# Kernel tuning notes

Hardware: AMD Instinct MI355X
Metric: run time of the kernel (lower is better)

## Reference

```python
import jax, jax.numpy as jnp
import numpy as np

NUM_HEADS = 8
NUM_GROUPS = 32
EPS = 1e-5


def setup_inputs() -> dict:
    key = jax.random.key(0)
    ks = jax.random.split(key, 12)
    B, C, H, W = 8, 512, 32, 32
    E = 512
    s = 1.0 / np.sqrt(C)
    inp = {
        "input_tensor": jax.random.normal(ks[0], (B, C, H, W), dtype=jnp.float32),
        "Wq": jax.random.normal(ks[1], (C, E), dtype=jnp.float32) * s,
        "bq": jnp.zeros((E,), dtype=jnp.float32),
        "Wk": jax.random.normal(ks[2], (C, E), dtype=jnp.float32) * s,
        "bk": jnp.zeros((E,), dtype=jnp.float32),
        "Wv": jax.random.normal(ks[3], (C, E), dtype=jnp.float32) * s,
        "bv": jnp.zeros((E,), dtype=jnp.float32),
        "Wo": jax.random.normal(ks[4], (E, E), dtype=jnp.float32) * s,
        "bo": jnp.zeros((E,), dtype=jnp.float32),
        "gamma": jnp.ones((E,), dtype=jnp.float32),
        "beta": jnp.zeros((E,), dtype=jnp.float32),
    }
    return inp


def reference(input_tensor, Wq, bq, Wk, bk, Wv, bv, Wo, bo, gamma, beta):
    B, C, H, W = input_tensor.shape
    E = Wq.shape[1]
    nH = NUM_HEADS
    hd = E // nH
    S = H * W

    # [B, C, H, W] -> [B, S, C]
    x = input_tensor.reshape(B, C, S).transpose(0, 2, 1)

    q = (x @ Wq + bq).reshape(B, S, nH, hd).transpose(0, 2, 1, 3)  # [B, h, S, d]
    k = (x @ Wk + bk).reshape(B, S, nH, hd).transpose(0, 2, 1, 3)
    v = (x @ Wv + bv).reshape(B, S, nH, hd).transpose(0, 2, 1, 3)

    scale = hd ** (-0.5)
    scores = jnp.einsum("bhqd,bhkd->bhqk", q, k) * scale
    weights = jax.nn.softmax(scores, axis=-1)
    attn = jnp.einsum("bhqk,bhkd->bhqd", weights, v)  # [B, h, S, d]

    attn = attn.transpose(0, 2, 1, 3).reshape(B, S, E)
    out = attn @ Wo + bo  # [B, S, E]
    out = out.transpose(0, 2, 1).reshape(B, E, H, W)

    y = out + input_tensor

    # GroupNorm over (channels_per_group, H, W)
    G = NUM_GROUPS
    yg = y.reshape(B, G, E // G, H, W)
    mean = jnp.mean(yg, axis=(2, 3, 4), keepdims=True)
    var = jnp.var(yg, axis=(2, 3, 4), keepdims=True)
    yn = ((yg - mean) * jax.lax.rsqrt(var + EPS)).reshape(B, E, H, W)
    return yn * gamma[None, :, None, None] + beta[None, :, None, None]
```

## Files before the change

kernel.cpp:

```cpp
#include <hip/hip_runtime.h>
#include <math.h>

constexpr int Bn  = 8;
constexpr int Cc  = 512;
constexpr int Ss  = 1024;
constexpr int Ee  = 512;
constexpr int nHd = 8;
constexpr int Hd  = 64;
constexpr int Gg  = 32;
constexpr int Cpg = 16;

typedef __bf16 bf16x8 __attribute__((ext_vector_type(8)));
typedef float  f32x4  __attribute__((ext_vector_type(4)));
typedef float  f32x16 __attribute__((ext_vector_type(16)));
typedef unsigned u32x4 __attribute__((ext_vector_type(4)));

__device__ inline __bf16 cvt_bf16(float f) {
    unsigned u = __builtin_bit_cast(unsigned, f);
    u += 0x7fffu + ((u >> 16) & 1u);
    unsigned short h = (unsigned short)(u >> 16);
    return __builtin_bit_cast(__bf16, h);
}

__device__ inline void gld16(const __bf16* g, __bf16* l) {
    __builtin_amdgcn_global_load_lds(
        (const __attribute__((address_space(1))) void*)g,
        (__attribute__((address_space(3))) void*)l, 16, 0, 0);
}

__device__ inline unsigned pk_bf16_rtz(float hi, float lo) {
    return __builtin_amdgcn_perm(__builtin_bit_cast(unsigned, hi),
                                 __builtin_bit_cast(unsigned, lo), 0x07060302u);
}

__global__ __launch_bounds__(256) void transpose_xw(
    const float* __restrict__ x, __bf16* __restrict__ xt,
    const float* __restrict__ w0, const float* __restrict__ w1,
    const float* __restrict__ w2, const float* __restrict__ w3,
    __bf16* __restrict__ d0, __bf16* __restrict__ d1,
    __bf16* __restrict__ d2, __bf16* __restrict__ d3,
    float* __restrict__ stats)
{
    __shared__ float T[32][33];
    const int r8 = threadIdx.x >> 5, c32 = threadIdx.x & 31;
    const int z = blockIdx.z;
    if (z < 8) {
        const int b = z, c0 = blockIdx.y * 32, s0 = blockIdx.x * 32;
#pragma unroll
        for (int i = 0; i < 4; i++)
            T[r8 + i * 8][c32] =
                x[((size_t)b * Cc + c0 + r8 + i * 8) * Ss + s0 + c32];
        __syncthreads();
#pragma unroll
        for (int i = 0; i < 4; i++)
            xt[((size_t)b * Ss + s0 + r8 + i * 8) * Cc + c0 + c32] =
                cvt_bf16(T[c32][r8 + i * 8]);
    } else {
        if (z == 8 && blockIdx.x == 0 && blockIdx.y == 0) {
            stats[threadIdx.x] = 0.0f;
            stats[threadIdx.x + 256] = 0.0f;
        }
        if (blockIdx.x >= 16) return;
        const int m = z - 8;
        const float* src = (m == 0) ? w0 : (m == 1) ? w1 : (m == 2) ? w2 : w3;
        __bf16* dst = (m == 0) ? d0 : (m == 1) ? d1 : (m == 2) ? d2 : d3;
        const int e0 = blockIdx.x * 32, c0 = blockIdx.y * 32;
#pragma unroll
        for (int i = 0; i < 4; i++)
            T[r8 + i * 8][c32] = src[(size_t)(c0 + r8 + i * 8) * Ee + e0 + c32];
        __syncthreads();
#pragma unroll
        for (int i = 0; i < 4; i++)
            dst[(size_t)(e0 + r8 + i * 8) * Cc + c0 + c32] =
                cvt_bf16(T[c32][r8 + i * 8]);
    }
}

__global__ __launch_bounds__(256) void qkv_mfma(
    const __bf16* __restrict__ xt,
    const __bf16* __restrict__ wqt, const __bf16* __restrict__ wkt,
    const __bf16* __restrict__ wvt,
    const float* __restrict__ bq, const float* __restrict__ bk,
    const float* __restrict__ bv,
    __bf16* __restrict__ qb, __bf16* __restrict__ kb, __bf16* __restrict__ vt)
{
    const int b = blockIdx.z;
    const int wsel = blockIdx.y >> 2;
    const int e0 = (blockIdx.y & 3) * 128;
    const int s0 = blockIdx.x * 128;
    const __bf16* A  = xt + (size_t)b * Ss * Cc;
    const __bf16* Bm = (wsel == 0) ? wqt : (wsel == 1) ? wkt : wvt;
    const float*  bias = (wsel == 0) ? bq : (wsel == 1) ? bk : bv;

    __shared__ __align__(16) char smem[128 * 136 * 2];
    __bf16* T = (__bf16*)smem;

    const int wave = threadIdx.x >> 6, lane = threadIdx.x & 63;
    const int lid = lane & 15, quad = lane >> 4;
    const int wm = wave & 1, wn = wave >> 1;
    const int srow = lane >> 2, sch = lane & 3;

    f32x4 acc[4][4] = {};

    auto stage = [&](int k0, int bufi) {
        __bf16* Asb = (__bf16*)(smem + bufi * 16384);
        __bf16* Bsb = (__bf16*)(smem + bufi * 16384 + 8192);
#pragma unroll
        for (int i = 0; i < 2; i++) {
            const int inst = wave * 2 + i;
            const int r = inst * 16 + srow;
            gld16(&A [(size_t)(s0 + r) * Cc + k0 + sch * 8], &Asb[inst * 512]);
            gld16(&Bm[(size_t)(e0 + r) * Cc + k0 + sch * 8], &Bsb[inst * 512]);
        }
    };

    stage(0, 0);
    for (int it = 0; it < 16; it++) {
        __syncthreads();
        if (it + 1 < 16) stage((it + 1) * 32, (it + 1) & 1);
        const __bf16* Asb = (const __bf16*)(smem + (it & 1) * 16384);
        const __bf16* Bsb = Asb + 4096;
        bf16x8 af[4], bf[4];
#pragma unroll
        for (int i = 0; i < 4; i++)
            af[i] = *(const bf16x8*)&Asb[(wm * 64 + i * 16 + lid) * 32 + quad * 8];
#pragma unroll
        for (int j = 0; j < 4; j++)
            bf[j] = *(const bf16x8*)&Bsb[(wn * 64 + j * 16 + lid) * 32 + quad * 8];
#pragma unroll
        for (int i = 0; i < 4; i++)
#pragma unroll
            for (int j = 0; j < 4; j++)
                acc[i][j] = __builtin_amdgcn_mfma_f32_16x16x32_bf16(
                    af[i], bf[j], acc[i][j], 0, 0, 0);
    }
    __syncthreads();

    float bj[4];
#pragma unroll
    for (int j = 0; j < 4; j++) bj[j] = bias[e0 + wn * 64 + j * 16 + lid];

    if (wsel == 2) {
#pragma unroll
        for (int i = 0; i < 4; i++) {
            const int s4 = wm * 64 + i * 16 + quad * 4;
#pragma unroll
            for (int j = 0; j < 4; j++) {
                const int e_l = wn * 64 + j * 16 + lid;
                unsigned short u0 = __builtin_bit_cast(unsigned short, cvt_bf16(acc[i][j][0] + bj[j]));
                unsigned short u1 = __builtin_bit_cast(unsigned short, cvt_bf16(acc[i][j][1] + bj[j]));
                unsigned short u2 = __builtin_bit_cast(unsigned short, cvt_bf16(acc[i][j][2] + bj[j]));
                unsigned short u3 = __builtin_bit_cast(unsigned short, cvt_bf16(acc[i][j][3] + bj[j]));
                uint2 pk;
                pk.x = (unsigned)u0 | ((unsigned)u1 << 16);
                pk.y = (unsigned)u2 | ((unsigned)u3 << 16);
                *(uint2*)&T[e_l * 136 + s4] = pk;
            }
        }
        __syncthreads();
        const int t = threadIdx.x;
#pragma unroll
        for (int it = 0; it < 8; it++) {
            const int idx = t + it * 256;
            const int e_l = idx >> 4, c8 = (idx & 15) * 8;
            bf16x8 val = *(const bf16x8*)&T[e_l * 136 + c8];
            const int e_g = e0 + e_l;
            const int head = e_g >> 6, d = e_g & 63;
            *(bf16x8*)&vt[(((size_t)b * nHd + head) * Hd + d) * Ss + s0 + c8] = val;
        }
    } else {
        __bf16* outp = (wsel == 0) ? qb : kb;
#pragma unroll
        for (int i = 0; i < 4; i++) {
#pragma unroll
            for (int j = 0; j < 4; j++) {
                const int e1 = e0 + wn * 64 + j * 16 + lid;
                const int head = e1 >> 6, d = e1 & 63;
#pragma unroll
                for (int r = 0; r < 4; r++) {
                    const int s1 = s0 + wm * 64 + i * 16 + quad * 4 + r;
                    outp[(((size_t)b * nHd + head) * Ss + s1) * Hd + d] =
                        cvt_bf16(acc[i][j][r] + bj[j]);
                }
            }
        }
    }
}

__global__ __launch_bounds__(256, 2) void attn_mfma(
    const __bf16* __restrict__ q, const __bf16* __restrict__ k,
    const __bf16* __restrict__ vt, __bf16* __restrict__ attn_out)
{
    const int bh = blockIdx.x;
    const int s0 = blockIdx.y * 128;
    const __bf16* qp = q  + (size_t)bh * Ss * Hd;
    const __bf16* kp = k  + (size_t)bh * Ss * Hd;
    const __bf16* vp = vt + (size_t)bh * Hd * Ss;

    __shared__ __align__(16) __bf16 Ks[2][128 * 64];
    __shared__ __align__(16) __bf16 Vs[2][64 * 128];

    const int wave = threadIdx.x >> 6, lane = threadIdx.x & 63;
    const int nl = lane & 31, h = lane >> 5;

    const int sq = s0 + wave * 32 + nl;
    bf16x8 qf[4];
#pragma unroll
    for (int kk2 = 0; kk2 < 4; kk2++)
        qf[kk2] = *(const bf16x8*)&qp[(size_t)sq * Hd + kk2 * 16 + h * 8];

    f32x16 oacc[2] = {};
    float rs = 0.0f;
    const float cexp = 0.125f * 1.44269504f;

    const int srow8 = lane >> 3, sch8 = lane & 7;
    const int srow4 = lane >> 4, sch16 = lane & 15;

    auto stageKV = [&](int kt, int bufi) {
        __bf16* Ksb = Ks[bufi];
        __bf16* Vsb = Vs[bufi];
#pragma unroll
        for (int i = 0; i < 4; i++) {
            const int inst = wave * 4 + i;
            const int rK = inst * 8 + srow8;
            gld16(&kp[(size_t)(kt * 128 + rK) * Hd + ((sch8 ^ (rK & 7)) * 8)],
                  &Ksb[inst * 512]);
            const int dR = inst * 4 + srow4;
            gld16(&vp[(size_t)dR * Ss + kt * 128 + ((sch16 ^ (dR & 15)) * 8)],
                  &Vsb[inst * 512]);
        }
    };

    stageKV(0, 0);
    for (int kt = 0; kt < 8; kt++) {
        __syncthreads();
        if (kt + 1 < 8) stageKV(kt + 1, (kt + 1) & 1);
        const __bf16* Ksb = Ks[kt & 1];
        const __bf16* Vsb = Vs[kt & 1];

        f32x16 sc[4] = {};
#pragma unroll
        for (int kk2 = 0; kk2 < 4; kk2++) {
#pragma unroll
            for (int mt = 0; mt < 4; mt++) {
                bf16x8 kf = *(const bf16x8*)&Ksb[(mt * 32 + nl) * 64 +
                                                 (((2 * kk2 + h) ^ (nl & 7)) * 8)];
                sc[mt] = __builtin_amdgcn_mfma_f32_32x32x16_bf16(
                    kf, qf[kk2], sc[mt], 0, 0, 0);
            }
        }

        unsigned frag[8][4];
#pragma unroll
        for (int mt = 0; mt < 4; mt++) {
            float p[16];
#pragma unroll
            for (int r = 0; r < 16; r++) {
                p[r] = __builtin_amdgcn_exp2f(sc[mt][r] * cexp);
                rs += p[r];
            }
            unsigned G[4][2];
#pragma unroll
            for (int qg = 0; qg < 4; qg++) {
                G[qg][0] = pk_bf16_rtz(p[4 * qg + 1], p[4 * qg + 0]);
                G[qg][1] = pk_bf16_rtz(p[4 * qg + 3], p[4 * qg + 2]);
            }
            const unsigned sA0 = h ? G[0][0] : G[1][0];
            const unsigned sA1 = h ? G[0][1] : G[1][1];
            const unsigned sB0 = h ? G[2][0] : G[3][0];
            const unsigned sB1 = h ? G[2][1] : G[3][1];
            const unsigned rA0 = __shfl_xor(sA0, 32, 64);
            const unsigned rA1 = __shfl_xor(sA1, 32, 64);
            const unsigned rB0 = __shfl_xor(sB0, 32, 64);
            const unsigned rB1 = __shfl_xor(sB1, 32, 64);
            frag[2 * mt][0]     = h ? rA0     : G[0][0];
            frag[2 * mt][1]     = h ? rA1     : G[0][1];
            frag[2 * mt][2]     = h ? G[1][0] : rA0;
            frag[2 * mt][3]     = h ? G[1][1] : rA1;
            frag[2 * mt + 1][0] = h ? rB0     : G[2][0];
            frag[2 * mt + 1][1] = h ? rB1     : G[2][1];
            frag[2 * mt + 1][2] = h ? G[3][0] : rB0;
            frag[2 * mt + 1][3] = h ? G[3][1] : rB1;
        }

#pragma unroll
        for (int kk = 0; kk < 8; kk++) {
            u32x4 fv = {frag[kk][0], frag[kk][1], frag[kk][2], frag[kk][3]};
            bf16x8 pf = __builtin_bit_cast(bf16x8, fv);
#pragma unroll
            for (int dt = 0; dt < 2; dt++) {
                bf16x8 vf = *(const bf16x8*)&Vsb[(dt * 32 + nl) * 128 +
                                                 (((kk * 2 + h) ^ (nl & 15)) * 8)];
                oacc[dt] = __builtin_amdgcn_mfma_f32_32x32x16_bf16(
                    pf, vf, oacc[dt], 0, 0, 0);
            }
        }
    }

    rs += __shfl_xor(rs, 32, 64);
    const float inv = 1.0f / rs;
    const int b = bh >> 3, head = bh & 7;
#pragma unroll
    for (int r = 0; r < 16; r++) {
        const int rowq = (r & 3) + 8 * (r >> 2) + 4 * h;
        const float invr = __shfl(inv, rowq, 64);
        const int s1 = s0 + wave * 32 + rowq;
#pragma unroll
        for (int dt = 0; dt < 2; dt++)
            attn_out[((size_t)b * Ss + s1) * Ee + head * Hd + dt * 32 + nl] =
                cvt_bf16(oacc[dt][r] * invr);
    }
}

__global__ __launch_bounds__(256) void outproj_mfma(
    const __bf16* __restrict__ attnb, const __bf16* __restrict__ wot,
    const float* __restrict__ bo, const float* __restrict__ xin,
    __bf16* __restrict__ y, float* __restrict__ stats)
{
    const int b  = blockIdx.z;
    const int e0 = blockIdx.y * 128;
    const int s0 = blockIdx.x * 128;
    const __bf16* Bm = attnb + (size_t)b * Ss * Ee;

    __shared__ __align__(16) char smem[32768];

    const int wave = threadIdx.x >> 6, lane = threadIdx.x & 63;
    const int lid = lane & 15, quad = lane >> 4;
    const int wm = wave & 1, wn = wave >> 1;
    const int srow = lane >> 2, sch = lane & 3;

    f32x4 acc[4][4] = {};

    auto stage = [&](int k0, int bufi) {
        __bf16* Asb = (__bf16*)(smem + bufi * 16384);
        __bf16* Bsb = (__bf16*)(smem + bufi * 16384 + 8192);
#pragma unroll
        for (int i = 0; i < 2; i++) {
            const int inst = wave * 2 + i;
            const int r = inst * 16 + srow;
            gld16(&wot[(size_t)(e0 + r) * Ee + k0 + sch * 8], &Asb[inst * 512]);
            gld16(&Bm [(size_t)(s0 + r) * Ee + k0 + sch * 8], &Bsb[inst * 512]);
        }
    };

    stage(0, 0);
    for (int it = 0; it < 16; it++) {
        __syncthreads();
        if (it + 1 < 16) stage((it + 1) * 32, (it + 1) & 1);
        const __bf16* Asb = (const __bf16*)(smem + (it & 1) * 16384);
        const __bf16* Bsb = Asb + 4096;
        bf16x8 af[4], bf[4];
#pragma unroll
        for (int i = 0; i < 4; i++)
            af[i] = *(const bf16x8*)&Asb[(wm * 64 + i * 16 + lid) * 32 + quad * 8];
#pragma unroll
        for (int j = 0; j < 4; j++)
            bf[j] = *(const bf16x8*)&Bsb[(wn * 64 + j * 16 + lid) * 32 + quad * 8];
#pragma unroll
        for (int i = 0; i < 4; i++)
#pragma unroll
            for (int j = 0; j < 4; j++)
                acc[i][j] = __builtin_amdgcn_mfma_f32_16x16x32_bf16(
                    af[i], bf[j], acc[i][j], 0, 0, 0);
    }

    float gs[4] = {}, gs2[4] = {};
#pragma unroll
    for (int i = 0; i < 4; i++) {
#pragma unroll
        for (int r = 0; r < 4; r++) {
            const int eo1 = e0 + wm * 64 + i * 16 + quad * 4 + r;
            const float bb = bo[eo1];
#pragma unroll
            for (int j = 0; j < 4; j++) {
                const int s1 = s0 + wn * 64 + j * 16 + lid;
                const size_t idx = ((size_t)b * Ee + eo1) * Ss + s1;
                const float v = acc[i][j][r] + bb + xin[idx];
                y[idx] = cvt_bf16(v);
                gs[i]  += v;
                gs2[i] += v * v;
            }
        }
    }
#pragma unroll
    for (int i = 0; i < 4; i++) {
        float a = gs[i], c = gs2[i];
#pragma unroll
        for (int off = 32; off > 0; off >>= 1) {
            a += __shfl_down(a, off, 64);
            c += __shfl_down(c, off, 64);
        }
        if (lane == 0) {
            const int g = (e0 >> 4) + wm * 4 + i;
            atomicAdd(&stats[(b * Gg + g) * 2 + 0], a);
            atomicAdd(&stats[(b * Gg + g) * 2 + 1], c);
        }
    }
}

__global__ __launch_bounds__(256) void gnorm_kernel(
    const __bf16* __restrict__ y, const float* __restrict__ gamma,
    const float* __restrict__ beta, const float* __restrict__ stats,
    float* __restrict__ out)
{
    const int bg = blockIdx.x;
    const int b = bg >> 5, g = bg & 31;
    const size_t base = ((size_t)b * Ee + g * Cpg) * Ss;
    const bf16x8* y8 = (const bf16x8*)(y + base);
    constexpr int N8 = (Cpg * Ss) / 8;
    constexpr float Nf = (float)(Cpg * Ss);

    const float mean = stats[bg * 2 + 0] / Nf;
    const float var  = stats[bg * 2 + 1] / Nf - mean * mean;
    const float rstd = rsqrtf(var + 1e-5f);

    for (int i = threadIdx.x; i < N8; i += 256) {
        bf16x8 vv = y8[i];
        const int c = g * Cpg + (i >> 7);
        const float gm = gamma[c] * rstd;
        const float bt = beta[c];
        f32x4 r0, r1;
#pragma unroll
        for (int j = 0; j < 4; j++) r0[j] = ((float)vv[j] - mean) * gm + bt;
#pragma unroll
        for (int j = 0; j < 4; j++) r1[j] = ((float)vv[4 + j] - mean) * gm + bt;
        *(f32x4*)&out[base + (size_t)i * 8]     = r0;
        *(f32x4*)&out[base + (size_t)i * 8 + 4] = r1;
    }
}

extern "C" void kernel_launch(void* const* d_in, const int* in_sizes, int n_in,
                              void* d_out, int out_size, void* d_ws, size_t ws_size,
                              hipStream_t stream)
{
    const float* x     = (const float*)d_in[0];
    const float* Wq    = (const float*)d_in[1];
    const float* bq    = (const float*)d_in[2];
    const float* Wk    = (const float*)d_in[3];
    const float* bk    = (const float*)d_in[4];
    const float* Wv    = (const float*)d_in[5];
    const float* bv    = (const float*)d_in[6];
    const float* Wo    = (const float*)d_in[7];
    const float* bo    = (const float*)d_in[8];
    const float* gamma = (const float*)d_in[9];
    const float* beta  = (const float*)d_in[10];
    float* out = (float*)d_out;

    char* ws = (char*)d_ws;
    __bf16* xt    = (__bf16*)ws;
    __bf16* wqt   = (__bf16*)(ws + (8u << 20));
    __bf16* wkt   = (__bf16*)(ws + (8u << 20) + (512u << 10));
    __bf16* wvt   = (__bf16*)(ws + (9u << 20));
    __bf16* wot   = (__bf16*)(ws + (9u << 20) + (512u << 10));
    __bf16* qb    = (__bf16*)(ws + (10u << 20));
    __bf16* kb    = (__bf16*)(ws + (18u << 20));
    __bf16* vtb   = (__bf16*)(ws + (26u << 20));
    __bf16* attnb = (__bf16*)(ws + (34u << 20));
    __bf16* yb    = (__bf16*)(ws + (42u << 20));
    float*  statb = (float*) (ws + (50u << 20));

    transpose_xw<<<dim3(32, 16, 12), 256, 0, stream>>>(
        x, xt, Wq, Wk, Wv, Wo, wqt, wkt, wvt, wot, statb);

    qkv_mfma<<<dim3(Ss / 128, 12, Bn), 256, 0, stream>>>(
        xt, wqt, wkt, wvt, bq, bk, bv, qb, kb, vtb);

    attn_mfma<<<dim3(Bn * nHd, Ss / 128), 256, 0, stream>>>(qb, kb, vtb, attnb);

    outproj_mfma<<<dim3(Ss / 128, Ee / 128, Bn), 256, 0, stream>>>(
        attnb, wot, bo, x, yb, statb);

    gnorm_kernel<<<Bn * Gg, 256, 0, stream>>>(yb, gamma, beta, statb, out);
}
```

Measured before the change: 155.9 us.

## Fuse GroupNorm into out-projection via grid-level counter barrier per group slice

The separate GroupNorm kernel and the bf16 intermediate y buffer are removed. Each out-projection block keeps its residual-added values in registers and atomically accumulates group statistics. It then waits on a per-(batch, channel-tile) counter until all 8 spatial blocks have contributed, reads the final mean and variance, and writes normalized fp32 output directly. This saves a full write and read of y plus one kernel launch. It relies on all 8 cooperating blocks being co-resident, since the spin-wait would deadlock otherwise; with 256 blocks that is likely but not guaranteed.

```diff
diff --git a/kernel.cpp b/kernel.cpp
--- a/kernel.cpp
+++ b/kernel.cpp
@@ -39,7 +39,7 @@
     const float* __restrict__ w2, const float* __restrict__ w3,
     __bf16* __restrict__ d0, __bf16* __restrict__ d1,
     __bf16* __restrict__ d2, __bf16* __restrict__ d3,
-    float* __restrict__ stats)
+    float* __restrict__ stats, unsigned* __restrict__ cnt)
 {
     __shared__ float T[32][33];
     const int r8 = threadIdx.x >> 5, c32 = threadIdx.x & 31;
@@ -59,6 +59,7 @@
         if (z == 8 && blockIdx.x == 0 && blockIdx.y == 0) {
             stats[threadIdx.x] = 0.0f;
             stats[threadIdx.x + 256] = 0.0f;
+            if (threadIdx.x < 32) cnt[threadIdx.x] = 0u;
         }
         if (blockIdx.x >= 16) return;
         const int m = z - 8;
@@ -312,10 +313,12 @@
     }
 }
 
-__global__ __launch_bounds__(256) void outproj_mfma(
+__global__ __launch_bounds__(256) void outproj_gnorm(
     const __bf16* __restrict__ attnb, const __bf16* __restrict__ wot,
     const float* __restrict__ bo, const float* __restrict__ xin,
-    __bf16* __restrict__ y, float* __restrict__ stats)
+    const float* __restrict__ gamma, const float* __restrict__ beta,
+    float* __restrict__ stats, unsigned* __restrict__ cnt,
+    float* __restrict__ out)
 {
     const int b  = blockIdx.z;
     const int e0 = blockIdx.y * 128;
@@ -376,7 +379,7 @@
                 const int s1 = s0 + wn * 64 + j * 16 + lid;
                 const size_t idx = ((size_t)b * Ee + eo1) * Ss + s1;
                 const float v = acc[i][j][r] + bb + xin[idx];
-                y[idx] = cvt_bf16(v);
+                acc[i][j][r] = v;
                 gs[i]  += v;
                 gs2[i] += v * v;
             }
@@ -396,36 +399,44 @@
             atomicAdd(&stats[(b * Gg + g) * 2 + 1], c);
         }
     }
-}
-
-__global__ __launch_bounds__(256) void gnorm_kernel(
-    const __bf16* __restrict__ y, const float* __restrict__ gamma,
-    const float* __restrict__ beta, const float* __restrict__ stats,
-    float* __restrict__ out)
-{
-    const int bg = blockIdx.x;
-    const int b = bg >> 5, g = bg & 31;
-    const size_t base = ((size_t)b * Ee + g * Cpg) * Ss;
-    const bf16x8* y8 = (const bf16x8*)(y + base);
-    constexpr int N8 = (Cpg * Ss) / 8;
+
+    __threadfence();
+    const int ci = b * 4 + (e0 >> 7);
+    if (threadIdx.x == 0) {
+        atomicAdd(&cnt[ci], 1u);
+        while (atomicAdd(&cnt[ci], 0u) < 8u) __builtin_amdgcn_s_sleep(2);
+    }
+    __syncthreads();
+
+    __shared__ float gmean[8], grstd[8];
     constexpr float Nf = (float)(Cpg * Ss);
-
-    const float mean = stats[bg * 2 + 0] / Nf;
-    const float var  = stats[bg * 2 + 1] / Nf - mean * mean;
-    const float rstd = rsqrtf(var + 1e-5f);
-
-    for (int i = threadIdx.x; i < N8; i += 256) {
-        bf16x8 vv = y8[i];
-        const int c = g * Cpg + (i >> 7);
-        const float gm = gamma[c] * rstd;
-        const float bt = beta[c];
-        f32x4 r0, r1;
-#pragma unroll
-        for (int j = 0; j < 4; j++) r0[j] = ((float)vv[j] - mean) * gm + bt;
-#pragma unroll
-        for (int j = 0; j < 4; j++) r1[j] = ((float)vv[4 + j] - mean) * gm + bt;
-        *(f32x4*)&out[base + (size_t)i * 8]     = r0;
-        *(f32x4*)&out[base + (size_t)i * 8 + 4] = r1;
+    if (threadIdx.x < 8) {
+        const int g = (e0 >> 4) + threadIdx.x;
+        const float sum = atomicAdd(&stats[(b * Gg + g) * 2 + 0], 0.0f);
+        const float sq  = atomicAdd(&stats[(b * Gg + g) * 2 + 1], 0.0f);
+        const float mean = sum / Nf;
+        const float var  = sq / Nf - mean * mean;
+        gmean[threadIdx.x] = mean;
+        grstd[threadIdx.x] = rsqrtf(var + 1e-5f);
+    }
+    __syncthreads();
+
+#pragma unroll
+    for (int i = 0; i < 4; i++) {
+        const float mean = gmean[wm * 4 + i];
+        const float rstd = grstd[wm * 4 + i];
+#pragma unroll
+        for (int r = 0; r < 4; r++) {
+            const int eo1 = e0 + wm * 64 + i * 16 + quad * 4 + r;
+            const float gm = gamma[eo1] * rstd;
+            const float bt = beta[eo1];
+#pragma unroll
+            for (int j = 0; j < 4; j++) {
+                const int s1 = s0 + wn * 64 + j * 16 + lid;
+                const size_t idx = ((size_t)b * Ee + eo1) * Ss + s1;
+                out[idx] = (acc[i][j][r] - mean) * gm + bt;
+            }
+        }
     }
 }
 
@@ -456,19 +467,17 @@
     __bf16* kb    = (__bf16*)(ws + (18u << 20));
     __bf16* vtb   = (__bf16*)(ws + (26u << 20));
     __bf16* attnb = (__bf16*)(ws + (34u << 20));
-    __bf16* yb    = (__bf16*)(ws + (42u << 20));
-    float*  statb = (float*) (ws + (50u << 20));
+    float*  statb = (float*) (ws + (42u << 20));
+    unsigned* cntb = (unsigned*)(ws + (42u << 20) + 2048);
 
     transpose_xw<<<dim3(32, 16, 12), 256, 0, stream>>>(
-        x, xt, Wq, Wk, Wv, Wo, wqt, wkt, wvt, wot, statb);
+        x, xt, Wq, Wk, Wv, Wo, wqt, wkt, wvt, wot, statb, cntb);
 
     qkv_mfma<<<dim3(Ss / 128, 12, Bn), 256, 0, stream>>>(
         xt, wqt, wkt, wvt, bq, bk, bv, qb, kb, vtb);
 
     attn_mfma<<<dim3(Bn * nHd, Ss / 128), 256, 0, stream>>>(qb, kb, vtb, attnb);
 
-    outproj_mfma<<<dim3(Ss / 128, Ee / 128, Bn), 256, 0, stream>>>(
-        attnb, wot, bo, x, yb, statb);
-
-    gnorm_kernel<<<Bn * Gg, 256, 0, stream>>>(yb, gamma, beta, statb, out);
-}
+    outproj_gnorm<<<dim3(Ss / 128, Ee / 128, Bn), 256, 0, stream>>>(
+        attnb, wot, bo, x, gamma, beta, statb, cntb, out);
+}
```

After: 174.8 us. 1.12x slower.

## Fuse Q/K/V projections into one 512-thread block sharing the X tile

Applied to the files above, without the earlier changes.

The QKV GEMM kernel now computes Q, K and V for the same 128x128 output tile in one block of 512 threads, instead of launching separate blocks per weight matrix. Each block stages the shared X tile once along with all three weight tiles, which removes the repeated reads of X and cuts the grid to a third of its former size. In exchange each block uses 64KB of shared memory and 96 accumulator registers per lane, which may lower occupancy. The block count drops from 768 to 256, which may hurt load balance across CUs.

```diff
diff --git a/kernel.cpp b/kernel.cpp
--- a/kernel.cpp
+++ b/kernel.cpp
@@ -76,7 +76,7 @@
     }
 }
 
-__global__ __launch_bounds__(256) void qkv_mfma(
+__global__ __launch_bounds__(512, 2) void qkv_mfma(
     const __bf16* __restrict__ xt,
     const __bf16* __restrict__ wqt, const __bf16* __restrict__ wkt,
     const __bf16* __restrict__ wvt,
@@ -84,33 +84,34 @@
     const float* __restrict__ bv,
     __bf16* __restrict__ qb, __bf16* __restrict__ kb, __bf16* __restrict__ vt)
 {
-    const int b = blockIdx.z;
-    const int wsel = blockIdx.y >> 2;
-    const int e0 = (blockIdx.y & 3) * 128;
+    const int b  = blockIdx.z;
+    const int e0 = blockIdx.y * 128;
     const int s0 = blockIdx.x * 128;
-    const __bf16* A  = xt + (size_t)b * Ss * Cc;
-    const __bf16* Bm = (wsel == 0) ? wqt : (wsel == 1) ? wkt : wvt;
-    const float*  bias = (wsel == 0) ? bq : (wsel == 1) ? bk : bv;
-
-    __shared__ __align__(16) char smem[128 * 136 * 2];
-    __bf16* T = (__bf16*)smem;
+    const __bf16* A = xt + (size_t)b * Ss * Cc;
+
+    __shared__ __align__(16) char smem[65536];
 
     const int wave = threadIdx.x >> 6, lane = threadIdx.x & 63;
     const int lid = lane & 15, quad = lane >> 4;
     const int wm = wave & 1, wn = wave >> 1;
     const int srow = lane >> 2, sch = lane & 3;
 
-    f32x4 acc[4][4] = {};
+    const int mat = wave >> 1;
+    const __bf16* msrc =
+        (mat == 0) ? (A   + (size_t)s0 * Cc) :
+        (mat == 1) ? (wqt + (size_t)e0 * Cc) :
+        (mat == 2) ? (wkt + (size_t)e0 * Cc) : (wvt + (size_t)e0 * Cc);
+    const int rbase = (wave & 1) * 64;
+
+    f32x4 acc[3][4][2] = {};
 
     auto stage = [&](int k0, int bufi) {
-        __bf16* Asb = (__bf16*)(smem + bufi * 16384);
-        __bf16* Bsb = (__bf16*)(smem + bufi * 16384 + 8192);
-#pragma unroll
-        for (int i = 0; i < 2; i++) {
-            const int inst = wave * 2 + i;
-            const int r = inst * 16 + srow;
-            gld16(&A [(size_t)(s0 + r) * Cc + k0 + sch * 8], &Asb[inst * 512]);
-            gld16(&Bm[(size_t)(e0 + r) * Cc + k0 + sch * 8], &Bsb[inst * 512]);
+        __bf16* base = (__bf16*)(smem + bufi * 32768);
+#pragma unroll
+        for (int i = 0; i < 4; i++) {
+            const int r = rbase + i * 16 + srow;
+            gld16(&msrc[(size_t)r * Cc + k0 + sch * 8],
+                  &base[(wave * 4 + i) * 512]);
         }
     };
 
@@ -118,69 +119,80 @@
     for (int it = 0; it < 16; it++) {
         __syncthreads();
         if (it + 1 < 16) stage((it + 1) * 32, (it + 1) & 1);
-        const __bf16* Asb = (const __bf16*)(smem + (it & 1) * 16384);
-        const __bf16* Bsb = Asb + 4096;
-        bf16x8 af[4], bf[4];
-#pragma unroll
-        for (int i = 0; i < 4; i++)
-            af[i] = *(const bf16x8*)&Asb[(wm * 64 + i * 16 + lid) * 32 + quad * 8];
-#pragma unroll
-        for (int j = 0; j < 4; j++)
-            bf[j] = *(const bf16x8*)&Bsb[(wn * 64 + j * 16 + lid) * 32 + quad * 8];
-#pragma unroll
-        for (int i = 0; i < 4; i++)
-#pragma unroll
-            for (int j = 0; j < 4; j++)
-                acc[i][j] = __builtin_amdgcn_mfma_f32_16x16x32_bf16(
-                    af[i], bf[j], acc[i][j], 0, 0, 0);
+        const __bf16* buf = (const __bf16*)(smem + (it & 1) * 32768);
+        bf16x8 af[4];
+#pragma unroll
+        for (int i = 0; i < 4; i++)
+            af[i] = *(const bf16x8*)&buf[(wm * 64 + i * 16 + lid) * 32 + quad * 8];
+#pragma unroll
+        for (int w = 0; w < 3; w++) {
+            const __bf16* Bs = buf + 4096 * (w + 1);
+            bf16x8 bf0 = *(const bf16x8*)&Bs[(wn * 32 + lid) * 32 + quad * 8];
+            bf16x8 bf1 = *(const bf16x8*)&Bs[(wn * 32 + 16 + lid) * 32 + quad * 8];
+#pragma unroll
+            for (int i = 0; i < 4; i++) {
+                acc[w][i][0] = __builtin_amdgcn_mfma_f32_16x16x32_bf16(
+                    af[i], bf0, acc[w][i][0], 0, 0, 0);
+                acc[w][i][1] = __builtin_amdgcn_mfma_f32_16x16x32_bf16(
+                    af[i], bf1, acc[w][i][1], 0, 0, 0);
+            }
+        }
     }
     __syncthreads();
 
-    float bj[4];
-#pragma unroll
-    for (int j = 0; j < 4; j++) bj[j] = bias[e0 + wn * 64 + j * 16 + lid];
-
-    if (wsel == 2) {
-#pragma unroll
-        for (int i = 0; i < 4; i++) {
-            const int s4 = wm * 64 + i * 16 + quad * 4;
-#pragma unroll
-            for (int j = 0; j < 4; j++) {
-                const int e_l = wn * 64 + j * 16 + lid;
-                unsigned short u0 = __builtin_bit_cast(unsigned short, cvt_bf16(acc[i][j][0] + bj[j]));
-                unsigned short u1 = __builtin_bit_cast(unsigned short, cvt_bf16(acc[i][j][1] + bj[j]));
-                unsigned short u2 = __builtin_bit_cast(unsigned short, cvt_bf16(acc[i][j][2] + bj[j]));
-                unsigned short u3 = __builtin_bit_cast(unsigned short, cvt_bf16(acc[i][j][3] + bj[j]));
-                uint2 pk;
-                pk.x = (unsigned)u0 | ((unsigned)u1 << 16);
-                pk.y = (unsigned)u2 | ((unsigned)u3 << 16);
-                *(uint2*)&T[e_l * 136 + s4] = pk;
-            }
-        }
-        __syncthreads();
+    const float* biasArr[3] = {bq, bk, bv};
+    float bj[3][2];
+#pragma unroll
+    for (int w = 0; w < 3; w++)
+#pragma unroll
+        for (int j = 0; j < 2; j++)
+            bj[w][j] = biasArr[w][e0 + wn * 32 + j * 16 + lid];
+
+    __bf16* T = (__bf16*)smem;
+#pragma unroll
+    for (int i = 0; i < 4; i++) {
+        const int s4 = wm * 64 + i * 16 + quad * 4;
+#pragma unroll
+        for (int j = 0; j < 2; j++) {
+            const int e_l = wn * 32 + j * 16 + lid;
+            unsigned short u0 = __builtin_bit_cast(unsigned short, cvt_bf16(acc[2][i][j][0] + bj[2][j]));
+            unsigned short u1 = __builtin_bit_cast(unsigned short, cvt_bf16(acc[2][i][j][1] + bj[2][j]));
+            unsigned short u2 = __builtin_bit_cast(unsigned short, cvt_bf16(acc[2][i][j][2] + bj[2][j]));
+            unsigned short u3 = __builtin_bit_cast(unsigned short, cvt_bf16(acc[2][i][j][3] + bj[2][j]));
+            uint2 pk;
+            pk.x = (unsigned)u0 | ((unsigned)u1 << 16);
+            pk.y = (unsigned)u2 | ((unsigned)u3 << 16);
+            *(uint2*)&T[e_l * 136 + s4] = pk;
+        }
+    }
+    __syncthreads();
+    {
         const int t = threadIdx.x;
 #pragma unroll
-        for (int it = 0; it < 8; it++) {
-            const int idx = t + it * 256;
+        for (int it2 = 0; it2 < 4; it2++) {
+            const int idx = t + it2 * 512;
             const int e_l = idx >> 4, c8 = (idx & 15) * 8;
             bf16x8 val = *(const bf16x8*)&T[e_l * 136 + c8];
             const int e_g = e0 + e_l;
             const int head = e_g >> 6, d = e_g & 63;
             *(bf16x8*)&vt[(((size_t)b * nHd + head) * Hd + d) * Ss + s0 + c8] = val;
         }
-    } else {
-        __bf16* outp = (wsel == 0) ? qb : kb;
+    }
+
+#pragma unroll
+    for (int w = 0; w < 2; w++) {
+        __bf16* outp = w ? kb : qb;
 #pragma unroll
         for (int i = 0; i < 4; i++) {
 #pragma unroll
-            for (int j = 0; j < 4; j++) {
-                const int e1 = e0 + wn * 64 + j * 16 + lid;
+            for (int j = 0; j < 2; j++) {
+                const int e1 = e0 + wn * 32 + j * 16 + lid;
                 const int head = e1 >> 6, d = e1 & 63;
 #pragma unroll
                 for (int r = 0; r < 4; r++) {
                     const int s1 = s0 + wm * 64 + i * 16 + quad * 4 + r;
                     outp[(((size_t)b * nHd + head) * Ss + s1) * Hd + d] =
-                        cvt_bf16(acc[i][j][r] + bj[j]);
+                        cvt_bf16(acc[w][i][j][r] + bj[w][j]);
                 }
             }
         }
@@ -462,7 +474,7 @@
     transpose_xw<<<dim3(32, 16, 12), 256, 0, stream>>>(
         x, xt, Wq, Wk, Wv, Wo, wqt, wkt, wvt, wot, statb);
 
-    qkv_mfma<<<dim3(Ss / 128, 12, Bn), 256, 0, stream>>>(
+    qkv_mfma<<<dim3(Ss / 128, Ee / 128, Bn), 512, 0, stream>>>(
         xt, wqt, wkt, wvt, bq, bk, bv, qb, kb, vtb);
 
     attn_mfma<<<dim3(Bn * nHd, Ss / 128), 256, 0, stream>>>(qb, kb, vtb, attnb);
```

After: 157.2 us. Within noise of the previous version (+0.8%).
